# Optimization experiments

Measured on AMD Instinct MI355X. Metric: run time of the kernel, lower is better.

Reference implementation:

```python
import jax, jax.numpy as jnp
import numpy as np

B, C_IN, C_OUT, L = 16, 512, 512, 2048
HEADS, K, U, KS, PAD = 4, 16, 1, 3, 1
VV = C_OUT // HEADS  # 128
EPS = 1e-5


def _conv1d(x, w, pad):
    # x: [B, Cin, L], w: [Cout, Cin, KS] -> [B, Cout, L]
    return jax.lax.conv_general_dilated(
        x, w, window_strides=(1,), padding=[(pad, pad)],
        dimension_numbers=('NCH', 'OIH', 'NCH'))


def _bn_eval(y, gamma, beta, mean, var):
    # inference-mode BatchNorm1d over channel axis
    scale = gamma * jax.lax.rsqrt(var + EPS)
    shift = beta - mean * scale
    return y * scale[None, :, None] + shift[None, :, None]


def setup_inputs() -> dict:
    key = jax.random.key(0)
    ks = jax.random.split(key, 8)
    std_q = 1.0 / np.sqrt(C_IN * KS)
    x = jax.random.normal(ks[0], (B, C_IN, L), dtype=jnp.float32)
    Wq = jax.random.normal(ks[1], (K * HEADS, C_IN, KS), dtype=jnp.float32) * std_q
    Wk = jax.random.normal(ks[2], (K * U, C_IN, KS), dtype=jnp.float32) * std_q
    Wv = jax.random.normal(ks[3], (VV * U, C_IN, KS), dtype=jnp.float32) * std_q
    embedding = jax.random.normal(ks[4], (K, U), dtype=jnp.float32)
    return {
        'x': x, 'Wq': Wq,
        'q_gamma': jnp.ones((K * HEADS,), jnp.float32),
        'q_beta': jnp.zeros((K * HEADS,), jnp.float32),
        'q_mean': jnp.zeros((K * HEADS,), jnp.float32),
        'q_var': jnp.ones((K * HEADS,), jnp.float32),
        'Wk': Wk, 'Wv': Wv,
        'v_gamma': jnp.ones((VV * U,), jnp.float32),
        'v_beta': jnp.zeros((VV * U,), jnp.float32),
        'v_mean': jnp.zeros((VV * U,), jnp.float32),
        'v_var': jnp.ones((VV * U,), jnp.float32),
        'embedding': embedding,
    }


def reference(x, Wq, q_gamma, q_beta, q_mean, q_var, Wk, Wv,
              v_gamma, v_beta, v_mean, v_var, embedding):
    batch, _, n = x.shape
    # projections
    q = _bn_eval(_conv1d(x, Wq, PAD), q_gamma, q_beta, q_mean, q_var)
    q = q.reshape(batch, HEADS, K, n)                      # bhkn
    keys = _conv1d(x, Wk, PAD).reshape(batch, K, U, n)     # bkun
    sm = jax.nn.softmax(keys, axis=-1)                     # softmax over positions
    v = _bn_eval(_conv1d(x, Wv, PAD), v_gamma, v_beta, v_mean, v_var)
    v = v.reshape(batch, VV, U, n)                         # bvun
    # content lambda
    lambda_c = jnp.einsum('bkun,bvun->bkv', sm, v)
    y_c = jnp.einsum('bhkn,bkv->bhvn', q, lambda_c)
    # position lambda
    lambda_p = jnp.einsum('ku,bvun->bkvn', embedding, v)
    y_p = jnp.einsum('bhkn,bkvn->bhvn', q, lambda_p)
    out = y_c + y_p
    return out.reshape(batch, HEADS * VV, n)
```

## Files before the change

kernel.cpp:

```cpp
#include <hip/hip_runtime.h>

#define BB 16
#define CIN 512
#define LLN 2048
#define EPSV 1e-5f

typedef __attribute__((ext_vector_type(8))) short bf16x8s;
typedef __attribute__((ext_vector_type(4))) float f32x4;

__device__ __forceinline__ unsigned short f2bf(float f) {
    union { float f; unsigned int i; } c; c.f = f;
    unsigned int x = c.i;
    unsigned int lsb = (x >> 16) & 1;
    x += 0x7fff + lsb;
    return (unsigned short)(x >> 16);
}
__device__ __forceinline__ unsigned int pack2bf(float a, float b) {
    return (unsigned int)f2bf(a) | ((unsigned int)f2bf(b) << 16);
}
__device__ __forceinline__ float bf2f(unsigned short u) {
    union { unsigned int i; float f; } c; c.i = ((unsigned int)u) << 16; return c.f;
}
__device__ __forceinline__ float bflo(unsigned int w) {
    union { unsigned int i; float f; } c; c.i = w << 16; return c.f;
}
__device__ __forceinline__ float bfhi(unsigned int w) {
    union { unsigned int i; float f; } c; c.i = w & 0xffff0000u; return c.f;
}

__device__ __forceinline__ void g2l16(const void* g, void* l) {
    typedef const __attribute__((address_space(1))) unsigned int GU;
    typedef __attribute__((address_space(3))) unsigned int LU;
    __builtin_amdgcn_global_load_lds((GU*)g, (LU*)l, 16, 0, 0);
}

#define WIMG_U16 6144

__global__ __launch_bounds__(256) void prep_all(
    const float* __restrict__ x,
    const float* __restrict__ Wq, const float* __restrict__ Wk,
    const float* __restrict__ Wv,
    unsigned short* __restrict__ xpk, unsigned short* __restrict__ Wpk)
{
    const int tid = threadIdx.x;
    if (blockIdx.z < 16) {
        __shared__ __align__(16) unsigned int xs[256 * 16];
        const int nt = blockIdx.x;
        const int c  = blockIdx.y;
        const int b  = blockIdx.z;
        const int n0 = nt * 256;
        const int p  = tid >> 4;
        const int ns = (tid & 15) * 4;
        const int g = p >> 2, pi = p & 3;
        const float* x0 = x + ((size_t)b * CIN + (size_t)(c * 32 + 2 * p)) * LLN + n0;
#pragma unroll
        for (int j = 0; j < 4; j++) {
            int nl = ns + j * 64;
            float4 a = *(const float4*)&x0[nl];
            float4 bq = *(const float4*)&x0[LLN + nl];
            int rp = n0 + nl + 1;
            xs[(nl + 0) * 16 + (g ^ (((rp + 0) >> 1) & 3)) * 4 + pi] = pack2bf(a.x, bq.x);
            xs[(nl + 1) * 16 + (g ^ (((rp + 1) >> 1) & 3)) * 4 + pi] = pack2bf(a.y, bq.y);
            xs[(nl + 2) * 16 + (g ^ (((rp + 2) >> 1) & 3)) * 4 + pi] = pack2bf(a.z, bq.z);
            xs[(nl + 3) * 16 + (g ^ (((rp + 3) >> 1) & 3)) * 4 + pi] = pack2bf(a.w, bq.w);
        }
        __syncthreads();
        uint4* dst = (uint4*)(xpk + ((size_t)(b * 16 + c) * 2050 + n0 + 1) * 32);
        const uint4* srcl = (const uint4*)xs;
#pragma unroll
        for (int k = 0; k < 4; k++)
            dst[tid + k * 256] = srcl[tid + k * 256];
        if (nt == 0 && tid < 4)
            *(uint4*)(xpk + ((size_t)(b * 16 + c) * 2050) * 32 + tid * 8) = make_uint4(0, 0, 0, 0);
        if (nt == 7 && tid < 4)
            *(uint4*)(xpk + ((size_t)(b * 16 + c) * 2050 + 2049) * 32 + tid * 8) = make_uint4(0, 0, 0, 0);
    } else {
        const int wblk = blockIdx.y * 8 + blockIdx.x;
        const int img = wblk >> 1, half = wblk & 1;
        const int cot = img >> 4, chunk = img & 15;
        const int ci0 = chunk * 32;
        for (int i = half * 3072 + tid; i < half * 3072 + 3072; i += 256) {
            int t = i >> 11, r = i & 2047;
            int cf = r >> 9, lane = (r >> 3) & 63, e = i & 7;
            int lm = lane & 15, kq = lane >> 4;
            int cop = cot * 64 + cf * 16 + lm;
            int cig = ci0 + kq * 8 + e;
            float val = 0.f;
            if (cop < 64)        val = Wq[((size_t)cop * 512 + cig) * 3 + t];
            else if (cop < 80)   val = Wk[((size_t)(cop - 64) * 512 + cig) * 3 + t];
            else if (cop < 208)  val = Wv[((size_t)(cop - 80) * 512 + cig) * 3 + t];
            Wpk[(size_t)img * WIMG_U16 + i] = f2bf(val);
        }
    }
}

__global__ __launch_bounds__(256) void conv_mfma(
    const unsigned short* __restrict__ xpk, const unsigned short* __restrict__ Wpk,
    const float* __restrict__ qg, const float* __restrict__ qb,
    const float* __restrict__ qm, const float* __restrict__ qv,
    const float* __restrict__ vg, const float* __restrict__ vb,
    const float* __restrict__ vm, const float* __restrict__ vvar,
    unsigned short* __restrict__ qb16, float* __restrict__ kbuf,
    unsigned short* __restrict__ vb16)
{
    __shared__ __align__(16) unsigned short xT[2][258 * 32];
    __shared__ __align__(16) unsigned short wA[2][WIMG_U16];
    __shared__ float sscale[64], sshift[64];

    const int tid = threadIdx.x;
    const int wave = tid >> 6, lane = tid & 63;
    const int kq = lane >> 4, lm = lane & 15;
    const int n0 = blockIdx.x * 256;
    const int cot = blockIdx.y;
    const int b = blockIdx.z;

    const unsigned short* xpanel = xpk + ((size_t)b * 16 * 2050 + n0) * 32;
    const unsigned short* wbase  = Wpk + (size_t)cot * 16 * WIMG_U16;

#define STAGE(buf, chunk)                                                      \
    {                                                                          \
        const unsigned short* wsrc = wbase + (size_t)(chunk) * WIMG_U16;       \
        const unsigned short* xsrc = xpanel + (size_t)(chunk) * 2050 * 32;     \
        for (int i = tid; i < 768; i += 256)  g2l16(wsrc + i * 8, &wA[buf][i * 8]); \
        for (int i = tid; i < 1032; i += 256) g2l16(xsrc + i * 8, &xT[buf][i * 8]); \
    }

    STAGE(0, 0)

    if (tid < 64) {
        int cop = cot * 64 + tid;
        float sc = 1.f, sh = 0.f;
        if (cop < 64) {
            float g = qg[cop], be = qb[cop], m = qm[cop], va = qv[cop];
            sc = g * rsqrtf(va + EPSV); sh = be - m * sc;
        } else if (cop >= 80 && cop < 208) {
            int cc = cop - 80;
            float g = vg[cc], be = vb[cc], m = vm[cc], va = vvar[cc];
            sc = g * rsqrtf(va + EPSV); sh = be - m * sc;
        }
        sscale[tid] = sc; sshift[tid] = sh;
    }

    f32x4 acc[4][4];
#pragma unroll
    for (int i = 0; i < 4; i++)
#pragma unroll
        for (int j = 0; j < 4; j++) acc[i][j] = (f32x4){0.f, 0.f, 0.f, 0.f};

    asm volatile("s_waitcnt vmcnt(0)" ::: "memory");
    __syncthreads();

    for (int chunk = 0; chunk < 16; chunk++) {
        const int cur = chunk & 1;
        if (chunk < 15) STAGE(cur ^ 1, chunk + 1)

#pragma unroll
        for (int t = 0; t < 3; t++) {
            bf16x8s aF[4];
#pragma unroll
            for (int cf = 0; cf < 4; cf++)
                aF[cf] = *(const bf16x8s*)&wA[cur][((t * 4 + cf) * 64 + lane) * 8];
#pragma unroll
            for (int fn = 0; fn < 4; fn++) {
                int lr = wave * 64 + fn * 16 + lm + t;
                int grp = kq ^ ((lr >> 1) & 3);
                bf16x8s bF = *(const bf16x8s*)&xT[cur][lr * 32 + grp * 8];
#pragma unroll
                for (int cf = 0; cf < 4; cf++)
                    acc[cf][fn] = __builtin_amdgcn_mfma_f32_16x16x32_bf16(
                        aF[cf], bF, acc[cf][fn], 0, 0, 0);
            }
        }
        asm volatile("s_waitcnt vmcnt(0)" ::: "memory");
        __syncthreads();
    }
#undef STAGE

#pragma unroll
    for (int cf = 0; cf < 4; cf++) {
#pragma unroll
        for (int fn = 0; fn < 4; fn++) {
#pragma unroll
            for (int r = 0; r < 4; r++) {
                int col = cf * 16 + kq * 4 + r;
                int cop = cot * 64 + col;
                if (cop >= 208) continue;
                float val = acc[cf][fn][r] * sscale[col] + sshift[col];
                int nout = n0 + wave * 64 + fn * 16 + lm;
                if (cop < 64)
                    qb16[((size_t)b * 64 + cop) * LLN + nout] = f2bf(val);
                else if (cop < 80)
                    kbuf[((size_t)b * 16 + (cop - 64)) * LLN + nout] = val;
                else
                    vb16[((size_t)b * 128 + (cop - 80)) * LLN + nout] = f2bf(val);
            }
        }
    }
}

__global__ __launch_bounds__(256) void lambdac_kernel(
    const float* __restrict__ kb, const unsigned short* __restrict__ vb16,
    float* __restrict__ lcb)
{
    const int wave = threadIdx.x >> 6;
    const int lane = threadIdx.x & 63;
    const int b = blockIdx.x >> 5;
    const int vg = blockIdx.x & 31;
    const float* ps = kb + ((size_t)b * 16 + wave * 4) * LLN;
    const unsigned short* pv = vb16 + ((size_t)b * 128 + vg * 4) * LLN;

    float m[4] = {-1e30f, -1e30f, -1e30f, -1e30f};
#pragma unroll
    for (int j = 0; j < 4; j++) {
        int n = (j * 64 + lane) * 8;
#pragma unroll
        for (int k = 0; k < 4; k++) {
            float4 a = *(const float4*)&ps[(size_t)k * LLN + n];
            float4 c = *(const float4*)&ps[(size_t)k * LLN + n + 4];
            m[k] = fmaxf(m[k], fmaxf(fmaxf(fmaxf(a.x, a.y), fmaxf(a.z, a.w)),
                                     fmaxf(fmaxf(c.x, c.y), fmaxf(c.z, c.w))));
        }
    }
#pragma unroll
    for (int k = 0; k < 4; k++)
#pragma unroll
        for (int off = 32; off > 0; off >>= 1)
            m[k] = fmaxf(m[k], __shfl_xor(m[k], off, 64));

    float sum[4] = {0.f, 0.f, 0.f, 0.f};
    float acc[4][4];
#pragma unroll
    for (int k = 0; k < 4; k++)
#pragma unroll
        for (int v = 0; v < 4; v++) acc[k][v] = 0.f;
#pragma unroll
    for (int j = 0; j < 4; j++) {
        int n = (j * 64 + lane) * 8;
        float e[4][8];
#pragma unroll
        for (int k = 0; k < 4; k++) {
            float4 a = *(const float4*)&ps[(size_t)k * LLN + n];
            float4 c = *(const float4*)&ps[(size_t)k * LLN + n + 4];
            e[k][0] = __expf(a.x - m[k]); e[k][1] = __expf(a.y - m[k]);
            e[k][2] = __expf(a.z - m[k]); e[k][3] = __expf(a.w - m[k]);
            e[k][4] = __expf(c.x - m[k]); e[k][5] = __expf(c.y - m[k]);
            e[k][6] = __expf(c.z - m[k]); e[k][7] = __expf(c.w - m[k]);
#pragma unroll
            for (int q = 0; q < 8; q++) sum[k] += e[k][q];
        }
#pragma unroll
        for (int v = 0; v < 4; v++) {
            uint4 w = *(const uint4*)&pv[(size_t)v * LLN + n];
            float vv[8] = {bflo(w.x), bfhi(w.x), bflo(w.y), bfhi(w.y),
                           bflo(w.z), bfhi(w.z), bflo(w.w), bfhi(w.w)};
#pragma unroll
            for (int k = 0; k < 4; k++) {
                float t = 0.f;
#pragma unroll
                for (int q = 0; q < 8; q++) t += e[k][q] * vv[q];
                acc[k][v] += t;
            }
        }
    }
#pragma unroll
    for (int k = 0; k < 4; k++) {
#pragma unroll
        for (int off = 32; off > 0; off >>= 1)
            sum[k] += __shfl_xor(sum[k], off, 64);
#pragma unroll
        for (int v = 0; v < 4; v++)
#pragma unroll
            for (int off = 32; off > 0; off >>= 1)
                acc[k][v] += __shfl_xor(acc[k][v], off, 64);
    }
    if (lane == 0) {
#pragma unroll
        for (int k = 0; k < 4; k++) {
            float inv = 1.f / sum[k];
#pragma unroll
            for (int v = 0; v < 4; v++)
                lcb[((size_t)b * 16 + wave * 4 + k) * 128 + vg * 4 + v] = acc[k][v] * inv;
        }
    }
}

__global__ __launch_bounds__(256) void final_kernel(
    const unsigned short* __restrict__ qb16, const unsigned short* __restrict__ vb16,
    const float* __restrict__ lcb, const float* __restrict__ emb,
    float* __restrict__ out)
{
    __shared__ float lcsT[128][16];
    __shared__ float es[16];
    const int tid = threadIdx.x;
    const int h = tid >> 6, nl = tid & 63;
    const int n0 = blockIdx.x * 64;
    const int b = blockIdx.y;

    for (int i = tid; i < 2048; i += 256)
        lcsT[i >> 4][i & 15] = lcb[(size_t)b * 2048 + (size_t)(i & 15) * 128 + (i >> 4)];
    if (tid < 16) es[tid] = emb[tid];
    __syncthreads();

    const int n = n0 + nl;
    const unsigned short* pq = qb16 + ((size_t)b * 64 + h * 16) * LLN + n;
    float4 q4[4];
#pragma unroll
    for (int kk = 0; kk < 4; kk++) {
        q4[kk].x = bf2f(pq[(size_t)(kk * 4 + 0) * LLN]);
        q4[kk].y = bf2f(pq[(size_t)(kk * 4 + 1) * LLN]);
        q4[kk].z = bf2f(pq[(size_t)(kk * 4 + 2) * LLN]);
        q4[kk].w = bf2f(pq[(size_t)(kk * 4 + 3) * LLN]);
    }
    float s = 0.f;
#pragma unroll
    for (int kk = 0; kk < 4; kk++)
        s += q4[kk].x * es[kk * 4] + q4[kk].y * es[kk * 4 + 1]
           + q4[kk].z * es[kk * 4 + 2] + q4[kk].w * es[kk * 4 + 3];

    const unsigned short* pv = vb16 + (size_t)b * 128 * LLN + n;
    float* po = out + ((size_t)b * 512 + h * 128) * LLN + n;
    for (int v = 0; v < 128; v++) {
        float4 c0 = *(const float4*)&lcsT[v][0];
        float4 c1 = *(const float4*)&lcsT[v][4];
        float4 c2 = *(const float4*)&lcsT[v][8];
        float4 c3 = *(const float4*)&lcsT[v][12];
        float lam = q4[0].x * c0.x + q4[0].y * c0.y + q4[0].z * c0.z + q4[0].w * c0.w
                  + q4[1].x * c1.x + q4[1].y * c1.y + q4[1].z * c1.z + q4[1].w * c1.w
                  + q4[2].x * c2.x + q4[2].y * c2.y + q4[2].z * c2.z + q4[2].w * c2.w
                  + q4[3].x * c3.x + q4[3].y * c3.y + q4[3].z * c3.z + q4[3].w * c3.w;
        float vvv = bf2f(pv[(size_t)v * LLN]);
        po[(size_t)v * LLN] = lam + s * vvv;
    }
}

extern "C" void kernel_launch(void* const* d_in, const int* in_sizes, int n_in,
                              void* d_out, int out_size, void* d_ws, size_t ws_size,
                              hipStream_t stream)
{
    const float* x   = (const float*)d_in[0];
    const float* Wq  = (const float*)d_in[1];
    const float* qg  = (const float*)d_in[2];
    const float* qb  = (const float*)d_in[3];
    const float* qm  = (const float*)d_in[4];
    const float* qv  = (const float*)d_in[5];
    const float* Wk  = (const float*)d_in[6];
    const float* Wv  = (const float*)d_in[7];
    const float* vg  = (const float*)d_in[8];
    const float* vb  = (const float*)d_in[9];
    const float* vm  = (const float*)d_in[10];
    const float* vva = (const float*)d_in[11];
    const float* emb = (const float*)d_in[12];
    float* out = (float*)d_out;

    float* kbuf = (float*)d_ws;
    float* lcb  = kbuf + (size_t)BB * 16 * LLN;
    unsigned short* qb16 = (unsigned short*)(lcb + (size_t)BB * 16 * 128);
    unsigned short* vb16 = qb16 + (size_t)BB * 64 * LLN;
    unsigned short* Wpk  = vb16 + (size_t)BB * 128 * LLN;
    unsigned short* xpk  = Wpk + (size_t)64 * WIMG_U16;

    hipLaunchKernelGGL(prep_all, dim3(8, 16, 17), dim3(256), 0, stream,
                       x, Wq, Wk, Wv, xpk, Wpk);

    hipLaunchKernelGGL(conv_mfma, dim3(8, 4, 16), dim3(256), 0, stream,
                       xpk, Wpk, qg, qb, qm, qv, vg, vb, vm, vva,
                       qb16, kbuf, vb16);

    hipLaunchKernelGGL(lambdac_kernel, dim3(512), dim3(256), 0, stream,
                       kbuf, vb16, lcb);

    hipLaunchKernelGGL(final_kernel, dim3(32, BB), dim3(256), 0, stream,
                       qb16, vb16, lcb, emb, out);
}
```

Baseline: 192.9 us.

## Halve conv position tile, load weights straight into registers, fix softmax shift

The conv kernel now covers 128 positions per block instead of 256. Weight fragments are read from global memory directly into registers rather than staged through LDS, which shrinks shared memory and sets a 4-block occupancy hint. This doubles the grid and raises occupancy, at the cost of redundant weight loads across blocks. The key projection is exponentiated in the conv epilogue with a fixed shift of 16 instead of the per-row max, so lambdac no longer needs its max pass or its exp calls; this can overflow or underflow if key values fall far outside the expected range. The final kernel's v loop is unrolled by 4.

```diff
diff --git a/kernel.cpp b/kernel.cpp
--- a/kernel.cpp
+++ b/kernel.cpp
@@ -94,7 +94,7 @@
     }
 }
 
-__global__ __launch_bounds__(256) void conv_mfma(
+__global__ __launch_bounds__(256, 4) void conv_mfma(
     const unsigned short* __restrict__ xpk, const unsigned short* __restrict__ Wpk,
     const float* __restrict__ qg, const float* __restrict__ qb,
     const float* __restrict__ qm, const float* __restrict__ qv,
@@ -103,29 +103,26 @@
     unsigned short* __restrict__ qb16, float* __restrict__ kbuf,
     unsigned short* __restrict__ vb16)
 {
-    __shared__ __align__(16) unsigned short xT[2][258 * 32];
-    __shared__ __align__(16) unsigned short wA[2][WIMG_U16];
+    __shared__ __align__(16) unsigned short xT[2][130 * 32];
     __shared__ float sscale[64], sshift[64];
 
     const int tid = threadIdx.x;
     const int wave = tid >> 6, lane = tid & 63;
     const int kq = lane >> 4, lm = lane & 15;
-    const int n0 = blockIdx.x * 256;
+    const int n0 = blockIdx.x * 128;
     const int cot = blockIdx.y;
     const int b = blockIdx.z;
 
     const unsigned short* xpanel = xpk + ((size_t)b * 16 * 2050 + n0) * 32;
-    const unsigned short* wbase  = Wpk + (size_t)cot * 16 * WIMG_U16;
-
-#define STAGE(buf, chunk)                                                      \
-    {                                                                          \
-        const unsigned short* wsrc = wbase + (size_t)(chunk) * WIMG_U16;       \
-        const unsigned short* xsrc = xpanel + (size_t)(chunk) * 2050 * 32;     \
-        for (int i = tid; i < 768; i += 256)  g2l16(wsrc + i * 8, &wA[buf][i * 8]); \
-        for (int i = tid; i < 1032; i += 256) g2l16(xsrc + i * 8, &xT[buf][i * 8]); \
-    }
-
-    STAGE(0, 0)
+    const unsigned short* wlane  = Wpk + (size_t)cot * 16 * WIMG_U16 + (size_t)lane * 8;
+
+#define STAGE_X(buf, chunk)                                                     \
+    {                                                                           \
+        const unsigned short* xsrc = xpanel + (size_t)(chunk) * 2050 * 32;      \
+        for (int i = tid; i < 520; i += 256) g2l16(xsrc + (size_t)i * 8, &xT[buf][i * 8]); \
+    }
+
+    STAGE_X(0, 0)
 
     if (tid < 64) {
         int cop = cot * 64 + tid;
@@ -141,56 +138,60 @@
         sscale[tid] = sc; sshift[tid] = sh;
     }
 
-    f32x4 acc[4][4];
+    f32x4 acc[4][2];
 #pragma unroll
     for (int i = 0; i < 4; i++)
 #pragma unroll
-        for (int j = 0; j < 4; j++) acc[i][j] = (f32x4){0.f, 0.f, 0.f, 0.f};
+        for (int j = 0; j < 2; j++) acc[i][j] = (f32x4){0.f, 0.f, 0.f, 0.f};
 
     asm volatile("s_waitcnt vmcnt(0)" ::: "memory");
     __syncthreads();
 
     for (int chunk = 0; chunk < 16; chunk++) {
         const int cur = chunk & 1;
-        if (chunk < 15) STAGE(cur ^ 1, chunk + 1)
+        const unsigned short* wc = wlane + (size_t)chunk * WIMG_U16;
+        bf16x8s aF[3][4];
+#pragma unroll
+        for (int t = 0; t < 3; t++)
+#pragma unroll
+            for (int cf = 0; cf < 4; cf++)
+                aF[t][cf] = *(const bf16x8s*)&wc[(t * 4 + cf) * 512];
+
+        if (chunk < 15) STAGE_X(cur ^ 1, chunk + 1)
 
 #pragma unroll
         for (int t = 0; t < 3; t++) {
-            bf16x8s aF[4];
-#pragma unroll
-            for (int cf = 0; cf < 4; cf++)
-                aF[cf] = *(const bf16x8s*)&wA[cur][((t * 4 + cf) * 64 + lane) * 8];
-#pragma unroll
-            for (int fn = 0; fn < 4; fn++) {
-                int lr = wave * 64 + fn * 16 + lm + t;
+#pragma unroll
+            for (int fn = 0; fn < 2; fn++) {
+                int lr = wave * 32 + fn * 16 + lm + t;
                 int grp = kq ^ ((lr >> 1) & 3);
                 bf16x8s bF = *(const bf16x8s*)&xT[cur][lr * 32 + grp * 8];
 #pragma unroll
                 for (int cf = 0; cf < 4; cf++)
                     acc[cf][fn] = __builtin_amdgcn_mfma_f32_16x16x32_bf16(
-                        aF[cf], bF, acc[cf][fn], 0, 0, 0);
+                        aF[t][cf], bF, acc[cf][fn], 0, 0, 0);
             }
         }
         asm volatile("s_waitcnt vmcnt(0)" ::: "memory");
         __syncthreads();
     }
-#undef STAGE
+#undef STAGE_X
 
 #pragma unroll
     for (int cf = 0; cf < 4; cf++) {
 #pragma unroll
-        for (int fn = 0; fn < 4; fn++) {
+        for (int fn = 0; fn < 2; fn++) {
 #pragma unroll
             for (int r = 0; r < 4; r++) {
                 int col = cf * 16 + kq * 4 + r;
                 int cop = cot * 64 + col;
                 if (cop >= 208) continue;
                 float val = acc[cf][fn][r] * sscale[col] + sshift[col];
-                int nout = n0 + wave * 64 + fn * 16 + lm;
+                int nout = n0 + wave * 32 + fn * 16 + lm;
                 if (cop < 64)
                     qb16[((size_t)b * 64 + cop) * LLN + nout] = f2bf(val);
                 else if (cop < 80)
-                    kbuf[((size_t)b * 16 + (cop - 64)) * LLN + nout] = val;
+                    kbuf[((size_t)b * 16 + (cop - 64)) * LLN + nout] = __expf(val - 16.f);
                 else
                     vb16[((size_t)b * 128 + (cop - 80)) * LLN + nout] = f2bf(val);
             }
@@ -199,54 +200,33 @@
 }
 
 __global__ __launch_bounds__(256) void lambdac_kernel(
-    const float* __restrict__ kb, const unsigned short* __restrict__ vb16,
+    const float* __restrict__ kexp, const unsigned short* __restrict__ vb16,
     float* __restrict__ lcb)
 {
     const int wave = threadIdx.x >> 6;
     const int lane = threadIdx.x & 63;
     const int b = blockIdx.x >> 5;
     const int vg = blockIdx.x & 31;
-    const float* ps = kb + ((size_t)b * 16 + wave * 4) * LLN;
+    const float* ps = kexp + ((size_t)b * 16 + wave * 4) * LLN;
     const unsigned short* pv = vb16 + ((size_t)b * 128 + vg * 4) * LLN;
 
-    float m[4] = {-1e30f, -1e30f, -1e30f, -1e30f};
+    float sum[4] = {0.f, 0.f, 0.f, 0.f};
+    float acc[4][4];
+#pragma unroll
+    for (int k = 0; k < 4; k++)
+#pragma unroll
+        for (int v = 0; v < 4; v++) acc[k][v] = 0.f;
 #pragma unroll
     for (int j = 0; j < 4; j++) {
         int n = (j * 64 + lane) * 8;
+        float e[4][8];
 #pragma unroll
         for (int k = 0; k < 4; k++) {
             float4 a = *(const float4*)&ps[(size_t)k * LLN + n];
             float4 c = *(const float4*)&ps[(size_t)k * LLN + n + 4];
-            m[k] = fmaxf(m[k], fmaxf(fmaxf(fmaxf(a.x, a.y), fmaxf(a.z, a.w)),
-                                     fmaxf(fmaxf(c.x, c.y), fmaxf(c.z, c.w))));
-        }
-    }
-#pragma unroll
-    for (int k = 0; k < 4; k++)
-#pragma unroll
-        for (int off = 32; off > 0; off >>= 1)
-            m[k] = fmaxf(m[k], __shfl_xor(m[k], off, 64));
-
-    float sum[4] = {0.f, 0.f, 0.f, 0.f};
-    float acc[4][4];
-#pragma unroll
-    for (int k = 0; k < 4; k++)
-#pragma unroll
-        for (int v = 0; v < 4; v++) acc[k][v] = 0.f;
-#pragma unroll
-    for (int j = 0; j < 4; j++) {
-        int n = (j * 64 + lane) * 8;
-        float e[4][8];
-#pragma unroll
-        for (int k = 0; k < 4; k++) {
-            float4 a = *(const float4*)&ps[(size_t)k * LLN + n];
-            float4 c = *(const float4*)&ps[(size_t)k * LLN + n + 4];
-            e[k][0] = __expf(a.x - m[k]); e[k][1] = __expf(a.y - m[k]);
-            e[k][2] = __expf(a.z - m[k]); e[k][3] = __expf(a.w - m[k]);
-            e[k][4] = __expf(c.x - m[k]); e[k][5] = __expf(c.y - m[k]);
-            e[k][6] = __expf(c.z - m[k]); e[k][7] = __expf(c.w - m[k]);
-#pragma unroll
-            for (int q = 0; q < 8; q++) sum[k] += e[k][q];
+            e[k][0] = a.x; e[k][1] = a.y; e[k][2] = a.z; e[k][3] = a.w;
+            e[k][4] = c.x; e[k][5] = c.y; e[k][6] = c.z; e[k][7] = c.w;
+            sum[k] += a.x + a.y + a.z + a.w + c.x + c.y + c.z + c.w;
         }
 #pragma unroll
         for (int v = 0; v < 4; v++) {
@@ -319,6 +299,7 @@
 
     const unsigned short* pv = vb16 + (size_t)b * 128 * LLN + n;
     float* po = out + ((size_t)b * 512 + h * 128) * LLN + n;
+#pragma unroll 4
     for (int v = 0; v < 128; v++) {
         float4 c0 = *(const float4*)&lcsT[v][0];
         float4 c1 = *(const float4*)&lcsT[v][4];
@@ -362,7 +343,7 @@
     hipLaunchKernelGGL(prep_all, dim3(8, 16, 17), dim3(256), 0, stream,
                        x, Wq, Wk, Wv, xpk, Wpk);
 
-    hipLaunchKernelGGL(conv_mfma, dim3(8, 4, 16), dim3(256), 0, stream,
+    hipLaunchKernelGGL(conv_mfma, dim3(16, 4, 16), dim3(256), 0, stream,
                        xpk, Wpk, qg, qb, qm, qv, vg, vb, vm, vva,
                        qb16, kbuf, vb16);
 
```

Measured after the change: 199.7 us. 1.03x slower.
